# Optimization experiments

Measured on AMD Instinct MI355X. Metric: run time of the kernel, lower is better.

## Reference

```python
import jax, jax.numpy as jnp
import numpy as np

B, T, E, H, L = 16, 512, 768, 12, 100
D = E // H
LN_EPS = 1e-12
NEG = -1e9


def setup_inputs() -> dict:
    key = jax.random.key(0)
    ks = jax.random.split(key, 12)
    s = 1.0 / np.sqrt(E)
    inp = {
        "last_hidden_states": jax.random.normal(ks[0], (B, T, E), jnp.float32),
        "att_mask": jnp.ones((B, T), jnp.float32),
        "type_emb": jax.random.normal(ks[1], (L, E), jnp.float32),
        # learned params
        "tp": jax.random.normal(ks[2], (E,), jnp.float32),
        "Wq": jax.random.normal(ks[3], (E, E), jnp.float32) * s,
        "bq": jnp.zeros((E,), jnp.float32),
        "Wk": jax.random.normal(ks[4], (E, E), jnp.float32) * s,
        "bk": jnp.zeros((E,), jnp.float32),
        "Wv": jax.random.normal(ks[5], (E, E), jnp.float32) * s,
        "bv": jnp.zeros((E,), jnp.float32),
        "Wo": jax.random.normal(ks[6], (E, E), jnp.float32) * s,
        "bo": jnp.zeros((E,), jnp.float32),
        "ln_g": jnp.ones((E,), jnp.float32),
        "ln_b": jnp.zeros((E,), jnp.float32),
    }
    return inp


def _layer_norm(x, g, b):
    mu = x.mean(-1, keepdims=True)
    var = ((x - mu) ** 2).mean(-1, keepdims=True)
    return (x - mu) * jax.lax.rsqrt(var + LN_EPS) * g + b


def reference(last_hidden_states, att_mask, type_emb, tp,
              Wq, bq, Wk, bk, Wv, bv, Wo, bo, ln_g, ln_b):
    b, t, e = last_hidden_states.shape
    # --- label cross-attention (no head split, no scaling) ---
    scores = jnp.einsum('bte,le->btl', last_hidden_states, type_emb)      # [b,t,l]
    att = jax.nn.softmax(scores, axis=-1)
    first_label_emb = jnp.einsum('btl,le->bte', att, type_emb)            # [b,t,e]

    h_truth = last_hidden_states + first_label_emb
    h_unknown = last_hidden_states + tp                                   # broadcast tp over [b,t]

    # --- two-stream masked self-attention: Q from unknown, K/V from truth,
    #     each position masked from attending to its own truth state ---
    q = (h_unknown @ Wq + bq).reshape(b, t, H, D)
    k = (h_truth @ Wk + bk).reshape(b, t, H, D)
    v = (h_truth @ Wv + bv).reshape(b, t, H, D)
    logits = jnp.einsum('bqhd,bkhd->bhqk', q, k) / np.sqrt(D).astype(np.float32)
    pad_bias = (1.0 - att_mask)[:, None, None, :] * NEG                   # [b,1,1,t]
    diag_bias = jnp.eye(t, dtype=logits.dtype)[None, None] * NEG          # [1,1,t,t]
    probs = jax.nn.softmax(logits + pad_bias + diag_bias, axis=-1)
    ctx = jnp.einsum('bhqk,bkhd->bqhd', probs, v).reshape(b, t, e)
    attn_out = ctx @ Wo + bo
    twice_hidden = _layer_norm(attn_out + h_unknown, ln_g, ln_b)

    out = twice_hidden + last_hidden_states + first_label_emb
    return out, scores
```

## Files before the change

### kernel.cpp

```cpp
#include <hip/hip_runtime.h>

typedef unsigned short u16;
typedef u16 u16x4 __attribute__((ext_vector_type(4)));
typedef u16 u16x8 __attribute__((ext_vector_type(8)));
typedef __bf16 bf16x8 __attribute__((ext_vector_type(8)));
typedef float f32x4 __attribute__((ext_vector_type(4)));

#define BB 16
#define TT 512
#define EE 768
#define HH 12
#define DD 64
#define LL 100
#define BT (BB*TT)
#define BTE ((size_t)BT*EE)
#define LOG2E 1.44269504f
#define QSCALE (0.125f*LOG2E)
#define FIXMAX 44.0f

__device__ __forceinline__ float bf2f(u16 u){
  union { float f; unsigned int i; } v; v.i = ((unsigned int)u) << 16; return v.f;
}
__device__ __forceinline__ u16 f2bf(float f){
  __bf16 h = (__bf16)f;
  union { __bf16 h; u16 u; } v; v.h = h; return v.u;
}

__device__ __forceinline__ void gload16(const u16* g, u16* l){
  __builtin_amdgcn_global_load_lds(
      (const __attribute__((address_space(1))) void*)g,
      (__attribute__((address_space(3))) void*)l, 16, 0, 0);
}

__global__ __launch_bounds__(256,1) void prep_all_kernel(
    const float* __restrict__ Wq, const float* __restrict__ Wk,
    const float* __restrict__ Wv, const float* __restrict__ Wo,
    u16* __restrict__ WT,
    const float* __restrict__ TE, u16* __restrict__ TEb, u16* __restrict__ TEt,
    const float* __restrict__ mask, float* __restrict__ MBg)
{
  __shared__ float tile[64][65];
  int bx = blockIdx.x;
  int tid = threadIdx.x;
  if (bx < 576){
    int m  = bx / 144, t = bx % 144;
    int tr = t / 12,  tc = t % 12;
    const float* W = (m==0)?Wq : (m==1)?Wk : (m==2)?Wv : Wo;
    u16* dst = WT + (size_t)m * EE * EE;
#pragma unroll
    for (int i=0;i<16;i++){
      int idx = tid + 256*i; int r = idx>>6, c = idx&63;
      tile[r][c] = W[(size_t)(tr*64+r)*EE + tc*64 + c];
    }
    __syncthreads();
#pragma unroll
    for (int i=0;i<16;i++){
      int idx = tid + 256*i; int r = idx>>6, c = idx&63;
      dst[(size_t)(tc*64+r)*EE + tr*64 + c] = f2bf(tile[c][r]);
    }
  } else if (bx < 960){
    int e = (bx - 576)*2 + (tid >> 7);
    int c = tid & 127;
    u16 v = 0;
    if (c < LL) v = f2bf(TE[(size_t)c*EE + e]);
    TEt[(size_t)e*128 + c] = v;
    if (e < 128){
#pragma unroll
      for (int k=c; k<EE; k+=128)
        TEb[(size_t)e*EE + k] = (e < LL) ? f2bf(TE[(size_t)e*EE + k]) : (u16)0;
    }
  } else {
    int i = (bx - 960)*256 + tid;
    MBg[i] = (1.0f - mask[i]) * (-1e9f * LOG2E) - FIXMAX;
  }
}

__global__ __launch_bounds__(64) void label_scores_kernel(
    const float* __restrict__ X, const u16* __restrict__ TEb,
    float* __restrict__ scores_out, u16* __restrict__ att)
{
  int m0 = blockIdx.x * 16;
  int lane = threadIdx.x;
  int l15 = lane & 15, g = lane >> 4;

  const float* xrow = X + (size_t)(m0 + l15)*EE;
  f32x4 s[7] = {};
  for (int k0=0; k0<EE; k0+=64){
    bf16x8 af[2];
#pragma unroll
    for (int kk=0;kk<2;kk++){
      const float* src = xrow + k0 + kk*32 + g*8;
      float4 a = *(const float4*)src, b = *(const float4*)(src+4);
      bf16x8 o;
      o[0]=(__bf16)a.x; o[1]=(__bf16)a.y; o[2]=(__bf16)a.z; o[3]=(__bf16)a.w;
      o[4]=(__bf16)b.x; o[5]=(__bf16)b.y; o[6]=(__bf16)b.z; o[7]=(__bf16)b.w;
      af[kk] = o;
    }
#pragma unroll
    for (int nt=0;nt<7;nt++){
      bf16x8 b0 = *(const bf16x8*)&TEb[(size_t)(nt*16+l15)*EE + k0 + g*8];
      bf16x8 b1 = *(const bf16x8*)&TEb[(size_t)(nt*16+l15)*EE + k0 + 32 + g*8];
      s[nt] = __builtin_amdgcn_mfma_f32_16x16x32_bf16(af[0], b0, s[nt], 0,0,0);
      s[nt] = __builtin_amdgcn_mfma_f32_16x16x32_bf16(af[1], b1, s[nt], 0,0,0);
    }
  }

  int rowb = m0 + g*4;
#pragma unroll
  for (int nt=0;nt<7;nt++){
    int col = nt*16 + l15;
    if (col < LL){
#pragma unroll
      for (int r=0;r<4;r++)
        scores_out[(size_t)(rowb + r)*LL + col] = s[nt][r];
    }
  }
  if (l15 >= 4){
#pragma unroll
    for (int r=0;r<4;r++) s[6][r] = -1e30f;
  }
  float inv[4];
#pragma unroll
  for (int r=0;r<4;r++){
    float tm = s[0][r];
#pragma unroll
    for (int nt=1;nt<7;nt++) tm = fmaxf(tm, s[nt][r]);
    tm = fmaxf(tm, __shfl_xor(tm, 1, 16));
    tm = fmaxf(tm, __shfl_xor(tm, 2, 16));
    tm = fmaxf(tm, __shfl_xor(tm, 4, 16));
    tm = fmaxf(tm, __shfl_xor(tm, 8, 16));
    float ps = 0.f;
#pragma unroll
    for (int nt=0;nt<7;nt++){
      float p = exp2f((s[nt][r] - tm) * LOG2E);
      s[nt][r] = p; ps += p;
    }
    ps += __shfl_xor(ps, 1, 16);
    ps += __shfl_xor(ps, 2, 16);
    ps += __shfl_xor(ps, 4, 16);
    ps += __shfl_xor(ps, 8, 16);
    inv[r] = 1.f/ps;
  }
#pragma unroll
  for (int nt=0;nt<7;nt++){
    int col = nt*16 + l15;
#pragma unroll
    for (int r=0;r<4;r++)
      att[(size_t)(rowb + r)*128 + col] = f2bf(s[nt][r] * inv[r]);
  }
  {
    int col = 112 + l15;
#pragma unroll
    for (int r=0;r<4;r++) att[(size_t)(rowb + r)*128 + col] = 0;
  }
}

__global__ __launch_bounds__(256,1) void gemm_fle_kernel(
    const u16* __restrict__ A, const u16* __restrict__ BTw,
    const float* __restrict__ Xf, const float* __restrict__ tp,
    u16* __restrict__ HT, u16* __restrict__ HU, int N, int K)
{
  __shared__ u16 As[128*40];
  __shared__ u16 Bs[128*40];
  int nb = N >> 7;
  int m0 = (blockIdx.x / nb) << 7;
  int n0 = (blockIdx.x % nb) << 7;
  int tid  = threadIdx.x, lane = tid & 63, w = tid >> 6;
  int wm = (w >> 1) << 6, wn = (w & 1) << 6;
  int lr = lane & 15, lk = (lane >> 4) << 3;

  f32x4 acc[4][4] = {};

  for (int k0 = 0; k0 < K; k0 += 32){
    __syncthreads();
#pragma unroll
    for (int i=0;i<2;i++){
      int idx = tid + (i<<8);
      int row = idx >> 2, kq = (idx & 3) << 3;
      *(u16x8*)&As[row*40 + kq] = *(const u16x8*)&A  [(size_t)(m0+row)*K + k0 + kq];
      *(u16x8*)&Bs[row*40 + kq] = *(const u16x8*)&BTw[(size_t)(n0+row)*K + k0 + kq];
    }
    __syncthreads();
    bf16x8 af[4], bfr[4];
#pragma unroll
    for (int i=0;i<4;i++) af [i] = *(const bf16x8*)&As[(wm + i*16 + lr)*40 + lk];
#pragma unroll
    for (int j=0;j<4;j++) bfr[j] = *(const bf16x8*)&Bs[(wn + j*16 + lr)*40 + lk];
#pragma unroll
    for (int i=0;i<4;i++)
#pragma unroll
      for (int j=0;j<4;j++)
        acc[i][j] = __builtin_amdgcn_mfma_f32_16x16x32_bf16(af[i], bfr[j], acc[i][j], 0, 0, 0);
  }

  int rbase = (lane >> 4) << 2;
#pragma unroll
  for (int j=0;j<4;j++){
    int col = n0 + wn + j*16 + lr;
    float tpv = tp[col];
#pragma unroll
    for (int i=0;i<4;i++){
#pragma unroll
      for (int r=0;r<4;r++){
        int row = m0 + wm + i*16 + rbase + r;
        float x = Xf[(size_t)row*EE + col];
        HT[(size_t)row*EE + col] = f2bf(x + acc[i][j][r]);
        HU[(size_t)row*EE + col] = f2bf(x + tpv);
      }
    }
  }
}

template<int NB, int FUSED>
__global__ __launch_bounds__(256,2) void gemm2_kernel(
    const u16* __restrict__ A0, const u16* __restrict__ A1,
    const u16* __restrict__ Wb,
    const float* __restrict__ b0, const float* __restrict__ b1,
    const float* __restrict__ b2,
    u16* __restrict__ C0, u16* __restrict__ C1, u16* __restrict__ C2)
{
  __shared__ u16 As[128*64];
  __shared__ u16 Bs[128*64];
  const int K = EE;

  int nwg = gridDim.x;
  int bid = blockIdx.x;
  int cpx = nwg >> 3;
  int swz = (bid & 7) * cpx + (bid >> 3);
  int mb = swz / NB, nb = swz % NB;
  int m0 = mb << 7;
  int n0 = (FUSED ? (nb % 6) : nb) << 7;

  int which = FUSED ? (nb / 6) : 0;
  const u16* Ap; const u16* Wp; const float* bp; u16* Cp;
  if (!FUSED){ Ap = A0; Wp = Wb; bp = b0; Cp = C0; }
  else {
    if (which == 0){ Ap = A0; Wp = Wb;                      bp = b0; Cp = C0; }
    else if (which == 1){ Ap = A1; Wp = Wb + (size_t)EE*EE; bp = b1; Cp = C1; }
    else { Ap = A1; Wp = Wb + 2*(size_t)EE*EE;              bp = b2; Cp = C2; }
  }

  int tid = threadIdx.x, lane = tid & 63, w = tid >> 6;
  int wm = (w >> 1) << 6, wn = (w & 1) << 6;
  int lr = lane & 15, g = lane >> 4;
  int lrow = lane >> 3;
  int lchunk = (lane & 7) ^ lrow;

  f32x4 acc[4][4] = {};

  for (int k0 = 0; k0 < K; k0 += 64){
    __syncthreads();
#pragma unroll
    for (int t=0;t<4;t++){
      int r0 = w*32 + t*8;
      gload16(&Ap[(size_t)(m0 + r0 + lrow)*K + k0 + (lchunk<<3)], &As[r0*64]);
      gload16(&Wp[(size_t)(n0 + r0 + lrow)*K + k0 + (lchunk<<3)], &Bs[r0*64]);
    }
    __syncthreads();
#pragma unroll
    for (int kk=0;kk<2;kk++){
      int cs = ((kk<<2) + g) ^ (lr & 7);
      bf16x8 af[4], bfr[4];
#pragma unroll
      for (int i=0;i<4;i++) af [i] = *(const bf16x8*)&As[(wm + i*16 + lr)*64 + (cs<<3)];
#pragma unroll
      for (int j=0;j<4;j++) bfr[j] = *(const bf16x8*)&Bs[(wn + j*16 + lr)*64 + (cs<<3)];
#pragma unroll
      for (int i=0;i<4;i++)
#pragma unroll
        for (int j=0;j<4;j++)
          acc[i][j] = __builtin_amdgcn_mfma_f32_16x16x32_bf16(af[i], bfr[j], acc[i][j], 0, 0, 0);
    }
  }

  int rbase = (lane >> 4) << 2;
  float scq = (FUSED && which==0) ? QSCALE : 1.0f;
#pragma unroll
  for (int j=0;j<4;j++){
    int col = n0 + wn + j*16 + lr;
    float bv = bp[col];
    if (FUSED && which == 2){
      int hh = col >> 6, d = col & 63;
#pragma unroll
      for (int i=0;i<4;i++){
        int row0 = m0 + wm + i*16 + rbase;
        int bb = row0 >> 9, t0 = row0 & 511;
        u16x4 o;
#pragma unroll
        for (int r=0;r<4;r++) o[r] = f2bf(acc[i][j][r] + bv);
        *(u16x4*)&Cp[((size_t)(bb*HH + hh)*DD + d)*TT + t0] = o;
      }
    } else {
#pragma unroll
      for (int i=0;i<4;i++){
#pragma unroll
        for (int r=0;r<4;r++){
          int row = m0 + wm + i*16 + rbase + r;
          Cp[(size_t)row*EE + col] = f2bf((acc[i][j][r] + bv) * scq);
        }
      }
    }
  }
}

__global__ __launch_bounds__(256,3) void attn_mfma_kernel(
    const u16* __restrict__ Q, const u16* __restrict__ K,
    const u16* __restrict__ VT, const float* __restrict__ MBg,
    u16* __restrict__ CTX)
{
  __shared__ u16 Ks [2][64*64];
  __shared__ u16 VTs[2][64*64];
  __shared__ u16 Pl [4][32*72];

  int bx = blockIdx.x;
  int bh = bx % (BB*HH), q0 = (bx / (BB*HH)) << 7;
  int b = bh / HH, h = bh % HH;
  int tid = threadIdx.x, lane = tid & 63, w = tid >> 6;
  int l15 = lane & 15, g = lane >> 4;
  int wq0 = q0 + w*32;
  size_t rowbase = (size_t)b*TT;
  u16* pw = &Pl[w][0];
  const u16* Kbh = K  + rowbase*EE + h*DD;
  const u16* Vbh = VT + (size_t)bh*DD*TT;
  int lrow = lane >> 3, lchunk = (lane & 7) ^ (lane >> 3);

  bf16x8 qf[2][2];
#pragma unroll
  for (int i=0;i<2;i++)
#pragma unroll
    for (int kk=0;kk<2;kk++)
      qf[i][kk] = *(const bf16x8*)&Q[(rowbase + wq0 + i*16 + l15)*EE + h*DD + kk*32 + g*8];

  f32x4 ctxf[2][4] = {};
  float lrun[2][4] = {};

#define STAGE(buf, k0)                                                          \
  { _Pragma("unroll")                                                           \
    for (int it=0; it<2; ++it){                                                 \
      int r0 = w*16 + it*8;                                                     \
      gload16(&Kbh[(size_t)((k0) + r0 + lrow)*EE + (lchunk<<3)], &Ks [buf][r0*64]); \
      gload16(&Vbh[(size_t)(r0 + lrow)*TT + (k0) + (lchunk<<3)], &VTs[buf][r0*64]); } }

  STAGE(0, 0);

  for (int kt=0; kt<8; ++kt){
    int k0 = kt << 6;
    int buf = kt & 1;
    __syncthreads();

    float mb[4];
#pragma unroll
    for (int kb=0;kb<4;kb++) mb[kb] = MBg[rowbase + k0 + kb*16 + l15];

    if (kt < 7) STAGE(buf^1, k0+64);

    f32x4 s[2][4] = {};
#pragma unroll
    for (int kk=0;kk<2;kk++){
      int cs = ((kk<<2) + g) ^ (l15 & 7);
      bf16x8 kf[4];
#pragma unroll
      for (int kb=0;kb<4;kb++)
        kf[kb] = *(const bf16x8*)&Ks[buf][(kb*16 + l15)*64 + (cs<<3)];
#pragma unroll
      for (int i=0;i<2;i++)
#pragma unroll
        for (int kb=0;kb<4;kb++)
          s[i][kb] = __builtin_amdgcn_mfma_f32_16x16x32_bf16(qf[i][kk], kf[kb], s[i][kb], 0,0,0);
    }

    if ((k0 < wq0 + 32) && (k0 + 64 > wq0)){
#pragma unroll
      for (int i=0;i<2;i++){
        int qr = wq0 + i*16 + g*4;
#pragma unroll
        for (int kb=0;kb<4;kb++){
          int kpos = k0 + kb*16 + l15;
#pragma unroll
          for (int r=0;r<4;r++)
            if (kpos == qr + r) s[i][kb][r] -= 1e9f*LOG2E;
        }
      }
    }

#pragma unroll
    for (int i=0;i<2;i++)
#pragma unroll
      for (int kb=0;kb<4;kb++)
#pragma unroll
        for (int r=0;r<4;r++){
          float p = exp2f(s[i][kb][r] + mb[kb]);
          lrun[i][r] += p;
          pw[(i*16 + g*4 + r)*72 + kb*16 + l15] = f2bf(p);
        }

    bf16x8 pa[2][2];
#pragma unroll
    for (int i=0;i<2;i++)
#pragma unroll
      for (int kk=0;kk<2;kk++)
        pa[i][kk] = *(const bf16x8*)&pw[(i*16 + l15)*72 + kk*32 + g*8];

#pragma unroll
    for (int kk=0;kk<2;kk++){
      int cs = ((kk<<2) + g) ^ (l15 & 7);
      bf16x8 vf[4];
#pragma unroll
      for (int dj=0;dj<4;dj++)
        vf[dj] = *(const bf16x8*)&VTs[buf][(dj*16 + l15)*64 + (cs<<3)];
#pragma unroll
      for (int i=0;i<2;i++)
#pragma unroll
        for (int dj=0;dj<4;dj++)
          ctxf[i][dj] = __builtin_amdgcn_mfma_f32_16x16x32_bf16(pa[i][kk], vf[dj], ctxf[i][dj], 0,0,0);
    }
  }
#undef STAGE

  float inv[2][4];
#pragma unroll
  for (int i=0;i<2;i++)
#pragma unroll
    for (int r=0;r<4;r++){
      float l = lrun[i][r];
      l += __shfl_xor(l, 1, 16);
      l += __shfl_xor(l, 2, 16);
      l += __shfl_xor(l, 4, 16);
      l += __shfl_xor(l, 8, 16);
      inv[i][r] = 1.0f / l;
    }
#pragma unroll
  for (int i=0;i<2;i++)
#pragma unroll
    for (int dj=0;dj<4;dj++)
#pragma unroll
      for (int r=0;r<4;r++)
        pw[(i*16 + g*4 + r)*64 + dj*16 + l15] = f2bf(ctxf[i][dj][r] * inv[i][r]);
#pragma unroll
  for (int t=0;t<4;t++){
    int row = lane >> 1, c = ((lane & 1)<<5) + t*8;
    *(u16x8*)&CTX[(rowbase + wq0 + row)*EE + h*DD + c] = *(const u16x8*)&pw[row*64 + c];
  }
}

__global__ __launch_bounds__(192,1) void ln_out_kernel(
    const u16* __restrict__ AO, const u16* __restrict__ HU,
    const u16* __restrict__ HT, const float* __restrict__ g,
    const float* __restrict__ bta, float* __restrict__ out)
{
  __shared__ float red[3];
  int r = blockIdx.x, tid = threadIdx.x;
  size_t base = (size_t)r*EE;
  int e0 = tid*4;
  u16x4 ao = *(const u16x4*)&AO[base+e0];
  u16x4 hu = *(const u16x4*)&HU[base+e0];
  u16x4 ht = *(const u16x4*)&HT[base+e0];
  float x[4];
#pragma unroll
  for (int j=0;j<4;j++) x[j] = bf2f(ao[j]) + bf2f(hu[j]);

  float s = x[0]+x[1]+x[2]+x[3];
#pragma unroll
  for (int o=32;o;o>>=1) s += __shfl_xor(s, o, 64);
  int w = tid>>6;
  if ((tid&63)==0) red[w] = s;
  __syncthreads();
  float mu = (red[0]+red[1]+red[2]) * (1.0f/EE);
  __syncthreads();
  float d2 = 0.f;
#pragma unroll
  for (int j=0;j<4;j++){ float d = x[j]-mu; d2 += d*d; }
#pragma unroll
  for (int o=32;o;o>>=1) d2 += __shfl_xor(d2, o, 64);
  if ((tid&63)==0) red[w] = d2;
  __syncthreads();
  float var = (red[0]+red[1]+red[2]) * (1.0f/EE);
  float rs = rsqrtf(var + 1e-12f);
  float4 gg = *(const float4*)&g[e0];
  float4 bb = *(const float4*)&bta[e0];
  float4 o4;
  o4.x = (x[0]-mu)*rs*gg.x + bb.x + bf2f(ht[0]);
  o4.y = (x[1]-mu)*rs*gg.y + bb.y + bf2f(ht[1]);
  o4.z = (x[2]-mu)*rs*gg.z + bb.z + bf2f(ht[2]);
  o4.w = (x[3]-mu)*rs*gg.w + bb.w + bf2f(ht[3]);
  *(float4*)&out[base+e0] = o4;
}

extern "C" void kernel_launch(void* const* d_in, const int* in_sizes, int n_in,
                              void* d_out, int out_size, void* d_ws, size_t ws_size,
                              hipStream_t stream)
{
  (void)in_sizes; (void)n_in; (void)out_size; (void)ws_size;
  const float* X    = (const float*)d_in[0];
  const float* mask = (const float*)d_in[1];
  const float* TE   = (const float*)d_in[2];
  const float* tp   = (const float*)d_in[3];
  const float* Wq   = (const float*)d_in[4];
  const float* bq   = (const float*)d_in[5];
  const float* Wk   = (const float*)d_in[6];
  const float* bk   = (const float*)d_in[7];
  const float* Wv   = (const float*)d_in[8];
  const float* bv   = (const float*)d_in[9];
  const float* Wo   = (const float*)d_in[10];
  const float* bo   = (const float*)d_in[11];
  const float* ln_g = (const float*)d_in[12];
  const float* ln_b = (const float*)d_in[13];

  float* out    = (float*)d_out;
  float* scores = out + BTE;

  char* ws = (char*)d_ws;
  const size_t BF = BTE*2;
  u16* HT   = (u16*)(ws);
  u16* HU   = (u16*)(ws + BF);
  u16* WT   = (u16*)(ws + 2*BF);
  u16* Qb   = (u16*)(ws + 2*BF + (size_t)4*EE*EE*2);
  u16* Kb   = Qb  + BTE;
  u16* VTb  = Kb  + BTE;
  u16* CTXb = VTb + BTE;
  u16* AOb  = CTXb + BTE;
  u16* ATT  = AOb + BTE;
  u16* TEb  = ATT + (size_t)BT*128;
  u16* TEt  = TEb + (size_t)128*EE;
  float* MBg = (float*)(TEt + (size_t)EE*128);

  prep_all_kernel<<<dim3(992), dim3(256), 0, stream>>>(
      Wq, Wk, Wv, Wo, WT, TE, TEb, TEt, mask, MBg);

  label_scores_kernel<<<dim3(BT/16), dim3(64), 0, stream>>>(X, TEb, scores, ATT);

  gemm_fle_kernel<<<dim3((BT/128)*(EE/128)), dim3(256), 0, stream>>>(
      ATT, TEt, X, tp, HT, HU, EE, 128);

  gemm2_kernel<18,1><<<dim3(64*18), dim3(256), 0, stream>>>(
      HU, HT, WT, bq, bk, bv, Qb, Kb, VTb);

  attn_mfma_kernel<<<dim3(BB*HH*4), dim3(256), 0, stream>>>(Qb, Kb, VTb, MBg, CTXb);

  gemm2_kernel<6,0><<<dim3(64*6), dim3(256), 0, stream>>>(
      CTXb, nullptr, WT + 3*(size_t)EE*EE, bo, nullptr, nullptr, AOb, nullptr, nullptr);

  ln_out_kernel<<<dim3(BT), dim3(192), 0, stream>>>(AOb, HU, HT, ln_g, ln_b, out);
}
```

Measured before the change: 139.4 us.

## Switch projection GEMMs and intermediates to FP8 storage and FP8 MFMA

Weights, the truth/unknown hidden states and the attention context are stored as FP8 instead of BF16. The QKV and output projections use FP8 MFMA with a K-tile of 128 bytes per stage, halving memory traffic and the number of K iterations. The residual paths in the final LayerNorm also read FP8 copies of the hidden states. The cost is a large precision loss in the output residuals and the projections, which may break the accuracy tolerance.

After: 119.9 us. 1.16x faster.

```diff
diff --git a/kernel.cpp b/kernel.cpp
--- a/kernel.cpp
+++ b/kernel.cpp
@@ -1,9 +1,11 @@
 #include <hip/hip_runtime.h>
 
+typedef unsigned char u8;
 typedef unsigned short u16;
 typedef u16 u16x4 __attribute__((ext_vector_type(4)));
 typedef u16 u16x8 __attribute__((ext_vector_type(8)));
 typedef __bf16 bf16x8 __attribute__((ext_vector_type(8)));
+typedef float f32x2 __attribute__((ext_vector_type(2)));
 typedef float f32x4 __attribute__((ext_vector_type(4)));
 
 #define BB 16
@@ -25,8 +27,14 @@
   __bf16 h = (__bf16)f;
   union { __bf16 h; u16 u; } v; v.h = h; return v.u;
 }
-
-__device__ __forceinline__ void gload16(const u16* g, u16* l){
+__device__ __forceinline__ u16 pk_fp8(float a, float b){
+  return (u16)(__builtin_amdgcn_cvt_pk_fp8_f32(a, b, 0, false) & 0xffff);
+}
+__device__ __forceinline__ u8 f2fp8(float a){
+  return (u8)(__builtin_amdgcn_cvt_pk_fp8_f32(a, 0.f, 0, false) & 0xff);
+}
+
+__device__ __forceinline__ void gload16(const void* g, void* l){
   __builtin_amdgcn_global_load_lds(
       (const __attribute__((address_space(1))) void*)g,
       (__attribute__((address_space(3))) void*)l, 16, 0, 0);
@@ -35,7 +43,7 @@
 __global__ __launch_bounds__(256,1) void prep_all_kernel(
     const float* __restrict__ Wq, const float* __restrict__ Wk,
     const float* __restrict__ Wv, const float* __restrict__ Wo,
-    u16* __restrict__ WT,
+    u8* __restrict__ WT8,
     const float* __restrict__ TE, u16* __restrict__ TEb, u16* __restrict__ TEt,
     const float* __restrict__ mask, float* __restrict__ MBg)
 {
@@ -46,7 +54,7 @@
     int m  = bx / 144, t = bx % 144;
     int tr = t / 12,  tc = t % 12;
     const float* W = (m==0)?Wq : (m==1)?Wk : (m==2)?Wv : Wo;
-    u16* dst = WT + (size_t)m * EE * EE;
+    u8* dst = WT8 + (size_t)m * EE * EE;
 #pragma unroll
     for (int i=0;i<16;i++){
       int idx = tid + 256*i; int r = idx>>6, c = idx&63;
@@ -54,9 +62,11 @@
     }
     __syncthreads();
 #pragma unroll
-    for (int i=0;i<16;i++){
-      int idx = tid + 256*i; int r = idx>>6, c = idx&63;
-      dst[(size_t)(tc*64+r)*EE + tr*64 + c] = f2bf(tile[c][r]);
+    for (int i=0;i<8;i++){
+      int idx = tid + 256*i;
+      int r = idx >> 5, cp = idx & 31;
+      u16 pk = pk_fp8(tile[cp*2][r], tile[cp*2+1][r]);
+      *(u16*)&dst[(size_t)(tc*64+r)*EE + tr*64 + cp*2] = pk;
     }
   } else if (bx < 960){
     int e = (bx - 576)*2 + (tid >> 7);
@@ -158,7 +168,7 @@
 __global__ __launch_bounds__(256,1) void gemm_fle_kernel(
     const u16* __restrict__ A, const u16* __restrict__ BTw,
     const float* __restrict__ Xf, const float* __restrict__ tp,
-    u16* __restrict__ HT, u16* __restrict__ HU, int N, int K)
+    u8* __restrict__ HT8, u8* __restrict__ HU8, int N, int K)
 {
   __shared__ u16 As[128*40];
   __shared__ u16 Bs[128*40];
@@ -204,23 +214,23 @@
       for (int r=0;r<4;r++){
         int row = m0 + wm + i*16 + rbase + r;
         float x = Xf[(size_t)row*EE + col];
-        HT[(size_t)row*EE + col] = f2bf(x + acc[i][j][r]);
-        HU[(size_t)row*EE + col] = f2bf(x + tpv);
+        HT8[(size_t)row*EE + col] = f2fp8(x + acc[i][j][r]);
+        HU8[(size_t)row*EE + col] = f2fp8(x + tpv);
       }
     }
   }
 }
 
 template<int NB, int FUSED>
-__global__ __launch_bounds__(256,2) void gemm2_kernel(
-    const u16* __restrict__ A0, const u16* __restrict__ A1,
-    const u16* __restrict__ Wb,
+__global__ __launch_bounds__(256,2) void gemm8_kernel(
+    const u8* __restrict__ A0, const u8* __restrict__ A1,
+    const u8* __restrict__ Wb,
     const float* __restrict__ b0, const float* __restrict__ b1,
     const float* __restrict__ b2,
     u16* __restrict__ C0, u16* __restrict__ C1, u16* __restrict__ C2)
 {
-  __shared__ u16 As[128*64];
-  __shared__ u16 Bs[128*64];
+  __shared__ __align__(16) u8 As[128*128];
+  __shared__ __align__(16) u8 Bs[128*128];
   const int K = EE;
 
   int nwg = gridDim.x;
@@ -232,7 +242,7 @@
   int n0 = (FUSED ? (nb % 6) : nb) << 7;
 
   int which = FUSED ? (nb / 6) : 0;
-  const u16* Ap; const u16* Wp; const float* bp; u16* Cp;
+  const u8* Ap; const u8* Wp; const float* bp; u16* Cp;
   if (!FUSED){ Ap = A0; Wp = Wb; bp = b0; Cp = C0; }
   else {
     if (which == 0){ Ap = A0; Wp = Wb;                      bp = b0; Cp = C0; }
@@ -248,28 +258,29 @@
 
   f32x4 acc[4][4] = {};
 
-  for (int k0 = 0; k0 < K; k0 += 64){
+  for (int k0 = 0; k0 < K; k0 += 128){
     __syncthreads();
 #pragma unroll
     for (int t=0;t<4;t++){
       int r0 = w*32 + t*8;
-      gload16(&Ap[(size_t)(m0 + r0 + lrow)*K + k0 + (lchunk<<3)], &As[r0*64]);
-      gload16(&Wp[(size_t)(n0 + r0 + lrow)*K + k0 + (lchunk<<3)], &Bs[r0*64]);
+      gload16(&Ap[(size_t)(m0 + r0 + lrow)*K + k0 + (lchunk<<4)], &As[r0*128]);
+      gload16(&Wp[(size_t)(n0 + r0 + lrow)*K + k0 + (lchunk<<4)], &Bs[r0*128]);
     }
     __syncthreads();
 #pragma unroll
-    for (int kk=0;kk<2;kk++){
-      int cs = ((kk<<2) + g) ^ (lr & 7);
-      bf16x8 af[4], bfr[4];
-#pragma unroll
-      for (int i=0;i<4;i++) af [i] = *(const bf16x8*)&As[(wm + i*16 + lr)*64 + (cs<<3)];
-#pragma unroll
-      for (int j=0;j<4;j++) bfr[j] = *(const bf16x8*)&Bs[(wn + j*16 + lr)*64 + (cs<<3)];
+    for (int kk=0;kk<4;kk++){
+      int cs  = ((kk<<1) + (g>>1)) ^ (lr & 7);
+      int off = (cs<<4) + ((g&1)<<3);
+      long af[4], bfr[4];
+#pragma unroll
+      for (int i=0;i<4;i++) af [i] = *(const long*)&As[(wm + i*16 + lr)*128 + off];
+#pragma unroll
+      for (int j=0;j<4;j++) bfr[j] = *(const long*)&Bs[(wn + j*16 + lr)*128 + off];
 #pragma unroll
       for (int i=0;i<4;i++)
 #pragma unroll
         for (int j=0;j<4;j++)
-          acc[i][j] = __builtin_amdgcn_mfma_f32_16x16x32_bf16(af[i], bfr[j], acc[i][j], 0, 0, 0);
+          acc[i][j] = __builtin_amdgcn_mfma_f32_16x16x32_fp8_fp8(af[i], bfr[j], acc[i][j], 0, 0, 0);
     }
   }
 
@@ -306,7 +317,7 @@
 __global__ __launch_bounds__(256,3) void attn_mfma_kernel(
     const u16* __restrict__ Q, const u16* __restrict__ K,
     const u16* __restrict__ VT, const float* __restrict__ MBg,
-    u16* __restrict__ CTX)
+    u8* __restrict__ CTX8)
 {
   __shared__ u16 Ks [2][64*64];
   __shared__ u16 VTs[2][64*64];
@@ -439,13 +450,17 @@
 #pragma unroll
   for (int t=0;t<4;t++){
     int row = lane >> 1, c = ((lane & 1)<<5) + t*8;
-    *(u16x8*)&CTX[(rowbase + wq0 + row)*EE + h*DD + c] = *(const u16x8*)&pw[row*64 + c];
+    const u16* pv = &pw[row*64 + c];
+    u16x4 o8;
+#pragma unroll
+    for (int e=0;e<4;e++) o8[e] = pk_fp8(bf2f(pv[2*e]), bf2f(pv[2*e+1]));
+    *(u16x4*)&CTX8[(rowbase + wq0 + row)*EE + h*DD + c] = o8;
   }
 }
 
 __global__ __launch_bounds__(192,1) void ln_out_kernel(
-    const u16* __restrict__ AO, const u16* __restrict__ HU,
-    const u16* __restrict__ HT, const float* __restrict__ g,
+    const u16* __restrict__ AO, const u8* __restrict__ HU8,
+    const u8* __restrict__ HT8, const float* __restrict__ g,
     const float* __restrict__ bta, float* __restrict__ out)
 {
   __shared__ float red[3];
@@ -453,11 +468,17 @@
   size_t base = (size_t)r*EE;
   int e0 = tid*4;
   u16x4 ao = *(const u16x4*)&AO[base+e0];
-  u16x4 hu = *(const u16x4*)&HU[base+e0];
-  u16x4 ht = *(const u16x4*)&HT[base+e0];
+  int hu4 = *(const int*)&HU8[base+e0];
+  int ht4 = *(const int*)&HT8[base+e0];
+  f32x2 hulo = __builtin_amdgcn_cvt_pk_f32_fp8(hu4, false);
+  f32x2 huhi = __builtin_amdgcn_cvt_pk_f32_fp8(hu4, true);
+  f32x2 htlo = __builtin_amdgcn_cvt_pk_f32_fp8(ht4, false);
+  f32x2 hthi = __builtin_amdgcn_cvt_pk_f32_fp8(ht4, true);
+  float huv[4] = {hulo[0], hulo[1], huhi[0], huhi[1]};
+  float htv[4] = {htlo[0], htlo[1], hthi[0], hthi[1]};
   float x[4];
 #pragma unroll
-  for (int j=0;j<4;j++) x[j] = bf2f(ao[j]) + bf2f(hu[j]);
+  for (int j=0;j<4;j++) x[j] = bf2f(ao[j]) + huv[j];
 
   float s = x[0]+x[1]+x[2]+x[3];
 #pragma unroll
@@ -479,10 +500,10 @@
   float4 gg = *(const float4*)&g[e0];
   float4 bb = *(const float4*)&bta[e0];
   float4 o4;
-  o4.x = (x[0]-mu)*rs*gg.x + bb.x + bf2f(ht[0]);
-  o4.y = (x[1]-mu)*rs*gg.y + bb.y + bf2f(ht[1]);
-  o4.z = (x[2]-mu)*rs*gg.z + bb.z + bf2f(ht[2]);
-  o4.w = (x[3]-mu)*rs*gg.w + bb.w + bf2f(ht[3]);
+  o4.x = (x[0]-mu)*rs*gg.x + bb.x + htv[0];
+  o4.y = (x[1]-mu)*rs*gg.y + bb.y + htv[1];
+  o4.z = (x[2]-mu)*rs*gg.z + bb.z + htv[2];
+  o4.w = (x[3]-mu)*rs*gg.w + bb.w + htv[3];
   *(float4*)&out[base+e0] = o4;
 }
 
@@ -509,36 +530,35 @@
   float* out    = (float*)d_out;
   float* scores = out + BTE;
 
-  char* ws = (char*)d_ws;
-  const size_t BF = BTE*2;
-  u16* HT   = (u16*)(ws);
-  u16* HU   = (u16*)(ws + BF);
-  u16* WT   = (u16*)(ws + 2*BF);
-  u16* Qb   = (u16*)(ws + 2*BF + (size_t)4*EE*EE*2);
-  u16* Kb   = Qb  + BTE;
-  u16* VTb  = Kb  + BTE;
-  u16* CTXb = VTb + BTE;
-  u16* AOb  = CTXb + BTE;
-  u16* ATT  = AOb + BTE;
-  u16* TEb  = ATT + (size_t)BT*128;
-  u16* TEt  = TEb + (size_t)128*EE;
-  float* MBg = (float*)(TEt + (size_t)EE*128);
+  char* p = (char*)d_ws;
+  u8*  HT8  = (u8*)p;  p += BTE;
+  u8*  HU8  = (u8*)p;  p += BTE;
+  u8*  CTX8 = (u8*)p;  p += BTE;
+  u8*  WT8  = (u8*)p;  p += (size_t)4*EE*EE;
+  u16* Qb   = (u16*)p; p += BTE*2;
+  u16* Kb   = (u16*)p; p += BTE*2;
+  u16* VTb  = (u16*)p; p += BTE*2;
+  u16* AOb  = (u16*)p; p += BTE*2;
+  u16* ATT  = (u16*)p; p += (size_t)BT*128*2;
+  u16* TEb  = (u16*)p; p += (size_t)128*EE*2;
+  u16* TEt  = (u16*)p; p += (size_t)EE*128*2;
+  float* MBg = (float*)p;
 
   prep_all_kernel<<<dim3(992), dim3(256), 0, stream>>>(
-      Wq, Wk, Wv, Wo, WT, TE, TEb, TEt, mask, MBg);
+      Wq, Wk, Wv, Wo, WT8, TE, TEb, TEt, mask, MBg);
 
   label_scores_kernel<<<dim3(BT/16), dim3(64), 0, stream>>>(X, TEb, scores, ATT);
 
   gemm_fle_kernel<<<dim3((BT/128)*(EE/128)), dim3(256), 0, stream>>>(
-      ATT, TEt, X, tp, HT, HU, EE, 128);
-
-  gemm2_kernel<18,1><<<dim3(64*18), dim3(256), 0, stream>>>(
-      HU, HT, WT, bq, bk, bv, Qb, Kb, VTb);
-
-  attn_mfma_kernel<<<dim3(BB*HH*4), dim3(256), 0, stream>>>(Qb, Kb, VTb, MBg, CTXb);
-
-  gemm2_kernel<6,0><<<dim3(64*6), dim3(256), 0, stream>>>(
-      CTXb, nullptr, WT + 3*(size_t)EE*EE, bo, nullptr, nullptr, AOb, nullptr, nullptr);
-
-  ln_out_kernel<<<dim3(BT), dim3(192), 0, stream>>>(AOb, HU, HT, ln_g, ln_b, out);
-}
+      ATT, TEt, X, tp, HT8, HU8, EE, 128);
+
+  gemm8_kernel<18,1><<<dim3(64*18), dim3(256), 0, stream>>>(
+      HU8, HT8, WT8, bq, bk, bv, Qb, Kb, VTb);
+
+  attn_mfma_kernel<<<dim3(BB*HH*4), dim3(256), 0, stream>>>(Qb, Kb, VTb, MBg, CTX8);
+
+  gemm8_kernel<6,0><<<dim3(64*6), dim3(256), 0, stream>>>(
+      CTX8, nullptr, WT8 + 3*(size_t)EE*EE, bo, nullptr, nullptr, AOb, nullptr, nullptr);
+
+  ln_out_kernel<<<dim3(BT), dim3(192), 0, stream>>>(AOb, HU8, HT8, ln_g, ln_b, out);
+}
```
